# Optimization experiments

Hardware: AMD Instinct MI355X
Metric: run time of the kernel (lower is better)

The kernel has to match this reference:

```python
import jax, jax.numpy as jnp
import numpy as np

# Intersection(mode='product'):
#   a_fk = a @ feats.T            # [Na, K]
#   b_fk = b @ feats.T            # [Nb, K]
#   mask = (a_fk[:,None,:] > 0) & (b_fk[None,:,:] > 0)
#   result = sum_k (a_fk[:,None,:] * b_fk[None,:,:]) * mask   # [Na, Nb]
# For the product op, (x*y)*[x>0 & y>0] == relu(x)*relu(y) elementwise
# (any term with a non-positive factor is zeroed either way), so the
# broadcast+mask+reduce collapses exactly into a GEMM over relu'd scores.

def setup_inputs() -> dict:
    key = jax.random.key(0)
    k1, k2, k3 = jax.random.split(key, 3)
    a = jax.random.normal(k1, (1024, 2048), dtype=jnp.float32)
    b = jax.random.normal(k2, (1024, 2048), dtype=jnp.float32)
    feats = jax.random.normal(k3, (128, 2048), dtype=jnp.float32)
    return {"a": a, "b": b, "feats": feats}

def reference(a, b, feats):
    a_fk = a @ feats.T            # [Na, K]
    b_fk = b @ feats.T            # [Nb, K]
    # masked product-intersection reduced over K; identical math to the
    # broadcast (Na, Nb, K) -> sum formulation of the torch module.
    return jnp.einsum('ak,bk->ab', jax.nn.relu(a_fk), jax.nn.relu(b_fk))
```

## Files before the change

### kernel.cpp

```cpp
#include <hip/hip_runtime.h>


typedef __attribute__((ext_vector_type(8))) __bf16 bf16x8;
typedef __attribute__((ext_vector_type(4))) __bf16 bf16x4;
typedef __attribute__((ext_vector_type(4))) float floatx4;

#define KD     2048
#define NF     128
#define NA     1024
#define NPART  8
#define KSL    256
#define FKN    (2048 * 128)

static __device__ inline bf16x8 cvt8(float4 u, float4 v) {
    bf16x8 s;
    s[0] = (__bf16)u.x; s[1] = (__bf16)u.y; s[2] = (__bf16)u.z; s[3] = (__bf16)u.w;
    s[4] = (__bf16)v.x; s[5] = (__bf16)v.y; s[6] = (__bf16)v.z; s[7] = (__bf16)v.w;
    return s;
}

static __device__ inline bf16x4 cvt4(float4 u) {
    bf16x4 s;
    s[0] = (__bf16)u.x; s[1] = (__bf16)u.y; s[2] = (__bf16)u.z; s[3] = (__bf16)u.w;
    return s;
}

__global__ __launch_bounds__(256) void gemm1_part8(const float* __restrict__ A,
                                                   const float* __restrict__ B,
                                                   const float* __restrict__ F,
                                                   float* __restrict__ part) {
    __shared__ __bf16 Xs[32 * 40];
    __shared__ __bf16 Fs[128 * 40];

    const int t    = threadIdx.x;
    const int m0   = blockIdx.x * 32;
    const int s    = blockIdx.y;
    const int k0   = s * KSL;
    const float* src = (m0 < NA) ? (A + (size_t)m0 * KD)
                                 : (B + (size_t)(m0 - NA) * KD);

    const int lane = t & 63;
    const int w    = t >> 6;
    const int ln   = lane & 15;
    const int quad = lane >> 4;
    const int q8   = quad * 8;

    floatx4 acc[2][2];
#pragma unroll
    for (int mt = 0; mt < 2; mt++)
#pragma unroll
        for (int nt = 0; nt < 2; nt++)
            acc[mt][nt] = (floatx4){0.f, 0.f, 0.f, 0.f};

    const int xrow = t >> 3, xcol = (t & 7) * 4;
    const int frow = t >> 1, fcol = (t & 1) * 16;
    const float* xp = src + (size_t)xrow * KD + (k0 + xcol);
    const float* fp = F   + (size_t)frow * KD + (k0 + fcol);

    float4 xu = *(const float4*)(xp + 0);
    float4 f0 = *(const float4*)(fp + 0);
    float4 f1 = *(const float4*)(fp + 4);
    float4 f2 = *(const float4*)(fp + 8);
    float4 f3 = *(const float4*)(fp + 12);

#pragma unroll
    for (int kk = 0; kk < KSL; kk += 32) {
        *(bf16x4*)&Xs[xrow * 40 + xcol]     = cvt4(xu);
        *(bf16x8*)&Fs[frow * 40 + fcol]     = cvt8(f0, f1);
        *(bf16x8*)&Fs[frow * 40 + fcol + 8] = cvt8(f2, f3);
        __syncthreads();

        if (kk + 32 < KSL) {
            xu = *(const float4*)(xp + kk + 32);
            f0 = *(const float4*)(fp + kk + 32);
            f1 = *(const float4*)(fp + kk + 36);
            f2 = *(const float4*)(fp + kk + 40);
            f3 = *(const float4*)(fp + kk + 44);
        }

        bf16x8 bfrag[2];
#pragma unroll
        for (int nt = 0; nt < 2; nt++)
            bfrag[nt] = *(const bf16x8*)&Fs[(w * 32 + nt * 16 + ln) * 40 + q8];
#pragma unroll
        for (int mt = 0; mt < 2; mt++) {
            bf16x8 af = *(const bf16x8*)&Xs[(mt * 16 + ln) * 40 + q8];
#pragma unroll
            for (int nt = 0; nt < 2; nt++)
                acc[mt][nt] = __builtin_amdgcn_mfma_f32_16x16x32_bf16(
                    af, bfrag[nt], acc[mt][nt], 0, 0, 0);
        }
        __syncthreads();
    }

    float* pdst = part + (size_t)s * FKN;
#pragma unroll
    for (int mt = 0; mt < 2; mt++)
#pragma unroll
        for (int nt = 0; nt < 2; nt++)
#pragma unroll
            for (int r = 0; r < 4; r++) {
                int row = m0 + mt * 16 + quad * 4 + r;
                int col = w * 32 + nt * 16 + ln;
                pdst[(size_t)row * NF + col] = acc[mt][nt][r];
            }
}

__global__ __launch_bounds__(256) void reduce_relu(const float* __restrict__ part,
                                                   __bf16* __restrict__ fkb) {
    int idx = blockIdx.x * 256 + threadIdx.x;
    size_t base = (size_t)idx * 4;
    float4 sum = make_float4(0.f, 0.f, 0.f, 0.f);
#pragma unroll
    for (int s = 0; s < NPART; s++) {
        float4 u = *(const float4*)(part + (size_t)s * FKN + base);
        sum.x += u.x; sum.y += u.y; sum.z += u.z; sum.w += u.w;
    }
    bf16x4 o;
    o[0] = (__bf16)fmaxf(sum.x, 0.f);
    o[1] = (__bf16)fmaxf(sum.y, 0.f);
    o[2] = (__bf16)fmaxf(sum.z, 0.f);
    o[3] = (__bf16)fmaxf(sum.w, 0.f);
    *(bf16x4*)(fkb + base) = o;
}

__global__ __launch_bounds__(256) void gemm2(const __bf16* __restrict__ fkb,
                                             float* __restrict__ out) {
    __shared__ __bf16 Ps[64 * 136];
    __shared__ __bf16 Qs[64 * 136];

    const int t    = threadIdx.x;
    const int i0   = blockIdx.y * 64;
    const int j0   = blockIdx.x * 64;
    const int lane = t & 63;
    const int w    = t >> 6;
    const int wm   = w & 1;
    const int wn   = w >> 1;
    const int ln   = lane & 15;
    const int quad = lane >> 4;
    const int q8   = quad * 8;

    const int prow = t >> 2, pcol = (t & 3) * 32;
    {
        const __bf16* p = fkb + (size_t)(i0 + prow) * NF + pcol;
        const __bf16* q = fkb + (size_t)(NA + j0 + prow) * NF + pcol;
#pragma unroll
        for (int c = 0; c < 32; c += 8) {
            *(bf16x8*)&Ps[prow * 136 + pcol + c] = *(const bf16x8*)(p + c);
            *(bf16x8*)&Qs[prow * 136 + pcol + c] = *(const bf16x8*)(q + c);
        }
    }
    __syncthreads();

    floatx4 acc[2][2];
#pragma unroll
    for (int mt = 0; mt < 2; mt++)
#pragma unroll
        for (int nt = 0; nt < 2; nt++)
            acc[mt][nt] = (floatx4){0.f, 0.f, 0.f, 0.f};

#pragma unroll
    for (int k0 = 0; k0 < 128; k0 += 32) {
        bf16x8 af[2], bf[2];
#pragma unroll
        for (int mt = 0; mt < 2; mt++)
            af[mt] = *(const bf16x8*)&Ps[(wm * 32 + mt * 16 + ln) * 136 + k0 + q8];
#pragma unroll
        for (int nt = 0; nt < 2; nt++)
            bf[nt] = *(const bf16x8*)&Qs[(wn * 32 + nt * 16 + ln) * 136 + k0 + q8];
#pragma unroll
        for (int mt = 0; mt < 2; mt++)
#pragma unroll
            for (int nt = 0; nt < 2; nt++)
                acc[mt][nt] = __builtin_amdgcn_mfma_f32_16x16x32_bf16(
                    af[mt], bf[nt], acc[mt][nt], 0, 0, 0);
    }

#pragma unroll
    for (int mt = 0; mt < 2; mt++)
#pragma unroll
        for (int nt = 0; nt < 2; nt++)
#pragma unroll
            for (int r = 0; r < 4; r++) {
                int row = i0 + wm * 32 + mt * 16 + quad * 4 + r;
                int col = j0 + wn * 32 + nt * 16 + ln;
                out[(size_t)row * 1024 + col] = acc[mt][nt][r];
            }
}

extern "C" void kernel_launch(void* const* d_in, const int* in_sizes, int n_in,
                              void* d_out, int out_size, void* d_ws, size_t ws_size,
                              hipStream_t stream) {
    const float* a     = (const float*)d_in[0];
    const float* b     = (const float*)d_in[1];
    const float* feats = (const float*)d_in[2];
    float* out = (float*)d_out;

    float*   part = (float*)d_ws;
    __bf16*  fkb  = (__bf16*)((char*)d_ws + (size_t)NPART * FKN * 4);

    gemm1_part8<<<dim3(64, NPART), 256, 0, stream>>>(a, b, feats, part);
    reduce_relu<<<256, 256, 0, stream>>>(part, fkb);
    gemm2<<<dim3(16, 16), 256, 0, stream>>>(fkb, out);
}
```

Measured before the change: 79.88 us.

## Fuse split-K reduction and ReLU into GEMM2 and widen GEMM1 k-step

Removes the separate reduce_relu kernel. GEMM2 now sums the 8 split-K partials, applies ReLU and converts to bf16 while staging its tiles into shared memory, which saves one launch and one global round-trip. In exchange every GEMM2 block re-reads fp32 partials for its rows and columns, and each partial is read 16 times across blocks instead of once, which raises L2 traffic. GEMM1 also doubles its per-iteration k-chunk from 32 to 64, halving the number of syncthreads at the cost of more registers for prefetch.

After: 85.81 us. 1.07x slower.

```diff
diff --git a/kernel.cpp b/kernel.cpp
--- a/kernel.cpp
+++ b/kernel.cpp
@@ -19,18 +19,12 @@
     return s;
 }
 
-static __device__ inline bf16x4 cvt4(float4 u) {
-    bf16x4 s;
-    s[0] = (__bf16)u.x; s[1] = (__bf16)u.y; s[2] = (__bf16)u.z; s[3] = (__bf16)u.w;
-    return s;
-}
-
 __global__ __launch_bounds__(256) void gemm1_part8(const float* __restrict__ A,
                                                    const float* __restrict__ B,
                                                    const float* __restrict__ F,
                                                    float* __restrict__ part) {
-    __shared__ __bf16 Xs[32 * 40];
-    __shared__ __bf16 Fs[128 * 40];
+    __shared__ __bf16 Xs[32 * 72];
+    __shared__ __bf16 Fs[128 * 72];
 
     const int t    = threadIdx.x;
     const int m0   = blockIdx.x * 32;
@@ -52,43 +46,47 @@
         for (int nt = 0; nt < 2; nt++)
             acc[mt][nt] = (floatx4){0.f, 0.f, 0.f, 0.f};
 
-    const int xrow = t >> 3, xcol = (t & 7) * 4;
-    const int frow = t >> 1, fcol = (t & 1) * 16;
+    const int xrow = t >> 3, xcol = (t & 7) * 8;
+    const int frow = t >> 1, fcol = (t & 1) * 32;
     const float* xp = src + (size_t)xrow * KD + (k0 + xcol);
     const float* fp = F   + (size_t)frow * KD + (k0 + fcol);
 
-    float4 xu = *(const float4*)(xp + 0);
-    float4 f0 = *(const float4*)(fp + 0);
-    float4 f1 = *(const float4*)(fp + 4);
-    float4 f2 = *(const float4*)(fp + 8);
-    float4 f3 = *(const float4*)(fp + 12);
+    float4 xa = *(const float4*)(xp + 0);
+    float4 xb = *(const float4*)(xp + 4);
+    float4 fa[8];
+#pragma unroll
+    for (int i = 0; i < 8; i++) fa[i] = *(const float4*)(fp + 4 * i);
 
 #pragma unroll
-    for (int kk = 0; kk < KSL; kk += 32) {
-        *(bf16x4*)&Xs[xrow * 40 + xcol]     = cvt4(xu);
-        *(bf16x8*)&Fs[frow * 40 + fcol]     = cvt8(f0, f1);
-        *(bf16x8*)&Fs[frow * 40 + fcol + 8] = cvt8(f2, f3);
+    for (int kk = 0; kk < KSL; kk += 64) {
+        *(bf16x8*)&Xs[xrow * 72 + xcol] = cvt8(xa, xb);
+#pragma unroll
+        for (int i = 0; i < 4; i++)
+            *(bf16x8*)&Fs[frow * 72 + fcol + 8 * i] = cvt8(fa[2 * i], fa[2 * i + 1]);
         __syncthreads();
 
-        if (kk + 32 < KSL) {
-            xu = *(const float4*)(xp + kk + 32);
-            f0 = *(const float4*)(fp + kk + 32);
-            f1 = *(const float4*)(fp + kk + 36);
-            f2 = *(const float4*)(fp + kk + 40);
-            f3 = *(const float4*)(fp + kk + 44);
+        if (kk + 64 < KSL) {
+            xa = *(const float4*)(xp + kk + 64);
+            xb = *(const float4*)(xp + kk + 68);
+#pragma unroll
+            for (int i = 0; i < 8; i++)
+                fa[i] = *(const float4*)(fp + kk + 64 + 4 * i);
         }
 
-        bf16x8 bfrag[2];
 #pragma unroll
-        for (int nt = 0; nt < 2; nt++)
-            bfrag[nt] = *(const bf16x8*)&Fs[(w * 32 + nt * 16 + ln) * 40 + q8];
-#pragma unroll
-        for (int mt = 0; mt < 2; mt++) {
-            bf16x8 af = *(const bf16x8*)&Xs[(mt * 16 + ln) * 40 + q8];
+        for (int sub = 0; sub < 64; sub += 32) {
+            bf16x8 bfrag[2];
 #pragma unroll
             for (int nt = 0; nt < 2; nt++)
-                acc[mt][nt] = __builtin_amdgcn_mfma_f32_16x16x32_bf16(
-                    af, bfrag[nt], acc[mt][nt], 0, 0, 0);
+                bfrag[nt] = *(const bf16x8*)&Fs[(w * 32 + nt * 16 + ln) * 72 + sub + q8];
+#pragma unroll
+            for (int mt = 0; mt < 2; mt++) {
+                bf16x8 af = *(const bf16x8*)&Xs[(mt * 16 + ln) * 72 + sub + q8];
+#pragma unroll
+                for (int nt = 0; nt < 2; nt++)
+                    acc[mt][nt] = __builtin_amdgcn_mfma_f32_16x16x32_bf16(
+                        af, bfrag[nt], acc[mt][nt], 0, 0, 0);
+            }
         }
         __syncthreads();
     }
@@ -106,26 +104,8 @@
             }
 }
 
-__global__ __launch_bounds__(256) void reduce_relu(const float* __restrict__ part,
-                                                   __bf16* __restrict__ fkb) {
-    int idx = blockIdx.x * 256 + threadIdx.x;
-    size_t base = (size_t)idx * 4;
-    float4 sum = make_float4(0.f, 0.f, 0.f, 0.f);
-#pragma unroll
-    for (int s = 0; s < NPART; s++) {
-        float4 u = *(const float4*)(part + (size_t)s * FKN + base);
-        sum.x += u.x; sum.y += u.y; sum.z += u.z; sum.w += u.w;
-    }
-    bf16x4 o;
-    o[0] = (__bf16)fmaxf(sum.x, 0.f);
-    o[1] = (__bf16)fmaxf(sum.y, 0.f);
-    o[2] = (__bf16)fmaxf(sum.z, 0.f);
-    o[3] = (__bf16)fmaxf(sum.w, 0.f);
-    *(bf16x4*)(fkb + base) = o;
-}
-
-__global__ __launch_bounds__(256) void gemm2(const __bf16* __restrict__ fkb,
-                                             float* __restrict__ out) {
+__global__ __launch_bounds__(256) void gemm2_fused(const float* __restrict__ part,
+                                                   float* __restrict__ out) {
     __shared__ __bf16 Ps[64 * 136];
     __shared__ __bf16 Qs[64 * 136];
 
@@ -140,15 +120,29 @@
     const int quad = lane >> 4;
     const int q8   = quad * 8;
 
-    const int prow = t >> 2, pcol = (t & 3) * 32;
-    {
-        const __bf16* p = fkb + (size_t)(i0 + prow) * NF + pcol;
-        const __bf16* q = fkb + (size_t)(NA + j0 + prow) * NF + pcol;
 #pragma unroll
-        for (int c = 0; c < 32; c += 8) {
-            *(bf16x8*)&Ps[prow * 136 + pcol + c] = *(const bf16x8*)(p + c);
-            *(bf16x8*)&Qs[prow * 136 + pcol + c] = *(const bf16x8*)(q + c);
+    for (int g = 0; g < 8; g++) {
+        const int idx4 = g * 256 + t;
+        const int row  = idx4 >> 5;
+        const int col  = (idx4 & 31) * 4;
+        const float* p = part + (size_t)(i0 + row) * NF + col;
+        const float* q = part + (size_t)(NA + j0 + row) * NF + col;
+        float4 sp = make_float4(0.f, 0.f, 0.f, 0.f);
+        float4 sq = make_float4(0.f, 0.f, 0.f, 0.f);
+#pragma unroll
+        for (int s = 0; s < NPART; s++) {
+            float4 u = *(const float4*)(p + (size_t)s * FKN);
+            float4 v = *(const float4*)(q + (size_t)s * FKN);
+            sp.x += u.x; sp.y += u.y; sp.z += u.z; sp.w += u.w;
+            sq.x += v.x; sq.y += v.y; sq.z += v.z; sq.w += v.w;
         }
+        bf16x4 op, oq;
+        op[0] = (__bf16)fmaxf(sp.x, 0.f); op[1] = (__bf16)fmaxf(sp.y, 0.f);
+        op[2] = (__bf16)fmaxf(sp.z, 0.f); op[3] = (__bf16)fmaxf(sp.w, 0.f);
+        oq[0] = (__bf16)fmaxf(sq.x, 0.f); oq[1] = (__bf16)fmaxf(sq.y, 0.f);
+        oq[2] = (__bf16)fmaxf(sq.z, 0.f); oq[3] = (__bf16)fmaxf(sq.w, 0.f);
+        *(bf16x4*)&Ps[row * 136 + col] = op;
+        *(bf16x4*)&Qs[row * 136 + col] = oq;
     }
     __syncthreads();
 
@@ -196,10 +190,8 @@
     const float* feats = (const float*)d_in[2];
     float* out = (float*)d_out;
 
-    float*   part = (float*)d_ws;
-    __bf16*  fkb  = (__bf16*)((char*)d_ws + (size_t)NPART * FKN * 4);
+    float* part = (float*)d_ws;
 
     gemm1_part8<<<dim3(64, NPART), 256, 0, stream>>>(a, b, feats, part);
-    reduce_relu<<<256, 256, 0, stream>>>(part, fkb);
-    gemm2<<<dim3(16, 16), 256, 0, stream>>>(fkb, out);
+    gemm2_fused<<<dim3(16, 16), 256, 0, stream>>>(part, out);
 }
```

## Fuse split-K reduction and ReLU into GEMM1 via last-block atomic counter

Applied to the files above, without the earlier changes.

Removes the separate reduce_relu kernel launch. Each GEMM1 block writes its partial and bumps a per-row-tile atomic counter. The last of the 8 K-split blocks for that tile reads the other partials, adds them to its registers, applies ReLU and writes bf16 output. This saves one launch and one pass over the partial buffer, but puts a serialized tail reduction on the last-arriving blocks and relies on a global counter that is reset at the end of each call.

After: 146.8 us. 83.8% more time.

```diff
diff --git a/kernel.cpp b/kernel.cpp
--- a/kernel.cpp
+++ b/kernel.cpp
@@ -12,6 +12,8 @@
 #define KSL    256
 #define FKN    (2048 * 128)
 
+__device__ int g_ctr[64];
+
 static __device__ inline bf16x8 cvt8(float4 u, float4 v) {
     bf16x8 s;
     s[0] = (__bf16)u.x; s[1] = (__bf16)u.y; s[2] = (__bf16)u.z; s[3] = (__bf16)u.w;
@@ -25,12 +27,14 @@
     return s;
 }
 
-__global__ __launch_bounds__(256) void gemm1_part8(const float* __restrict__ A,
-                                                   const float* __restrict__ B,
-                                                   const float* __restrict__ F,
-                                                   float* __restrict__ part) {
+__global__ __launch_bounds__(256) void gemm1_red(const float* __restrict__ A,
+                                                 const float* __restrict__ B,
+                                                 const float* __restrict__ F,
+                                                 float* __restrict__ part,
+                                                 __bf16* __restrict__ fkb) {
     __shared__ __bf16 Xs[32 * 40];
     __shared__ __bf16 Fs[128 * 40];
+    __shared__ int s_old;
 
     const int t    = threadIdx.x;
     const int m0   = blockIdx.x * 32;
@@ -104,24 +108,42 @@
                 int col = w * 32 + nt * 16 + ln;
                 pdst[(size_t)row * NF + col] = acc[mt][nt][r];
             }
-}
-
-__global__ __launch_bounds__(256) void reduce_relu(const float* __restrict__ part,
-                                                   __bf16* __restrict__ fkb) {
-    int idx = blockIdx.x * 256 + threadIdx.x;
-    size_t base = (size_t)idx * 4;
-    float4 sum = make_float4(0.f, 0.f, 0.f, 0.f);
-#pragma unroll
-    for (int s = 0; s < NPART; s++) {
-        float4 u = *(const float4*)(part + (size_t)s * FKN + base);
-        sum.x += u.x; sum.y += u.y; sum.z += u.z; sum.w += u.w;
-    }
-    bf16x4 o;
-    o[0] = (__bf16)fmaxf(sum.x, 0.f);
-    o[1] = (__bf16)fmaxf(sum.y, 0.f);
-    o[2] = (__bf16)fmaxf(sum.z, 0.f);
-    o[3] = (__bf16)fmaxf(sum.w, 0.f);
-    *(bf16x4*)(fkb + base) = o;
+
+    __threadfence();
+    if (t == 0)
+        s_old = __hip_atomic_fetch_add(&g_ctr[blockIdx.x], 1,
+                                       __ATOMIC_ACQ_REL, __HIP_MEMORY_SCOPE_AGENT);
+    __syncthreads();
+
+    if (s_old == NPART - 1) {
+        __threadfence();
+#pragma unroll
+        for (int s2 = 0; s2 < NPART; s2++) {
+            if (s2 == s) continue;
+            const float* ps = part + (size_t)s2 * FKN;
+#pragma unroll
+            for (int mt = 0; mt < 2; mt++)
+#pragma unroll
+                for (int nt = 0; nt < 2; nt++)
+#pragma unroll
+                    for (int r = 0; r < 4; r++) {
+                        int row = m0 + mt * 16 + quad * 4 + r;
+                        int col = w * 32 + nt * 16 + ln;
+                        acc[mt][nt][r] += ps[(size_t)row * NF + col];
+                    }
+        }
+#pragma unroll
+        for (int mt = 0; mt < 2; mt++)
+#pragma unroll
+            for (int nt = 0; nt < 2; nt++)
+#pragma unroll
+                for (int r = 0; r < 4; r++) {
+                    int row = m0 + mt * 16 + quad * 4 + r;
+                    int col = w * 32 + nt * 16 + ln;
+                    fkb[(size_t)row * NF + col] = (__bf16)fmaxf(acc[mt][nt][r], 0.f);
+                }
+        if (t == 0) atomicExch(&g_ctr[blockIdx.x], 0);
+    }
 }
 
 __global__ __launch_bounds__(256) void gemm2(const __bf16* __restrict__ fkb,
@@ -199,7 +221,6 @@
     float*   part = (float*)d_ws;
     __bf16*  fkb  = (__bf16*)((char*)d_ws + (size_t)NPART * FKN * 4);
 
-    gemm1_part8<<<dim3(64, NPART), 256, 0, stream>>>(a, b, feats, part);
-    reduce_relu<<<256, 256, 0, stream>>>(part, fkb);
+    gemm1_red<<<dim3(64, NPART), 256, 0, stream>>>(a, b, feats, part, fkb);
     gemm2<<<dim3(16, 16), 256, 0, stream>>>(fkb, out);
 }
```

## Fuse split-K reduction and ReLU into the first GEMM with in-block K split

Applied to the files above, without the earlier changes.

Replaces the 8-way grid split-K first GEMM and its separate reduce/ReLU kernel with one kernel. Each 512-thread block computes 16 rows over the full K. Its four wave-pairs each take a K sub-slice, and the partial sums are reduced through shared memory before ReLU and the bf16 store. This drops the fp32 partial buffer round-trip through global memory and one kernel launch. In exchange the grid shrinks to 128 blocks, fewer than the CU count, and every block re-reads the whole feats matrix, which raises L2 traffic and may leave the kernel latency-bound.

Result: slower. 111.8 us (+39.9%).

```diff
diff --git a/kernel.cpp b/kernel.cpp
--- a/kernel.cpp
+++ b/kernel.cpp
@@ -5,12 +5,9 @@
 typedef __attribute__((ext_vector_type(4))) __bf16 bf16x4;
 typedef __attribute__((ext_vector_type(4))) float floatx4;
 
-#define KD     2048
-#define NF     128
-#define NA     1024
-#define NPART  8
-#define KSL    256
-#define FKN    (2048 * 128)
+#define KD   2048
+#define NF   128
+#define NA   1024
 
 static __device__ inline bf16x8 cvt8(float4 u, float4 v) {
     bf16x8 s;
@@ -25,103 +22,87 @@
     return s;
 }
 
-__global__ __launch_bounds__(256) void gemm1_part8(const float* __restrict__ A,
+__global__ __launch_bounds__(512) void gemm1_block(const float* __restrict__ A,
                                                    const float* __restrict__ B,
                                                    const float* __restrict__ F,
-                                                   float* __restrict__ part) {
-    __shared__ __bf16 Xs[32 * 40];
-    __shared__ __bf16 Fs[128 * 40];
+                                                   __bf16* __restrict__ fkb) {
+    __shared__ __attribute__((aligned(16))) __bf16 smem[(16 + 128) * 136];
+    __bf16* Xs = smem;
+    __bf16* Fs = smem + 16 * 136;
 
     const int t    = threadIdx.x;
-    const int m0   = blockIdx.x * 32;
-    const int s    = blockIdx.y;
-    const int k0   = s * KSL;
+    const int m0   = blockIdx.x * 16;
     const float* src = (m0 < NA) ? (A + (size_t)m0 * KD)
                                  : (B + (size_t)(m0 - NA) * KD);
 
     const int lane = t & 63;
     const int w    = t >> 6;
+    const int wf   = w & 1;
+    const int wk   = w >> 1;
     const int ln   = lane & 15;
     const int quad = lane >> 4;
     const int q8   = quad * 8;
+    const int kb   = wk * 32;
 
-    floatx4 acc[2][2];
+    floatx4 acc[4];
 #pragma unroll
-    for (int mt = 0; mt < 2; mt++)
+    for (int nt = 0; nt < 4; nt++) acc[nt] = (floatx4){0.f, 0.f, 0.f, 0.f};
+
+    const int xrow = t >> 5, xcol = (t & 31) * 4;
+    const int frow = t >> 2, fcol = (t & 3) * 32;
+    const float* xp = src + (size_t)xrow * KD + xcol;
+    const float* fp = F   + (size_t)frow * KD + fcol;
+
+    float4 xu = *(const float4*)(xp);
+    float4 fa[8];
 #pragma unroll
-        for (int nt = 0; nt < 2; nt++)
-            acc[mt][nt] = (floatx4){0.f, 0.f, 0.f, 0.f};
+    for (int i = 0; i < 8; i++) fa[i] = *(const float4*)(fp + 4 * i);
 
-    const int xrow = t >> 3, xcol = (t & 7) * 4;
-    const int frow = t >> 1, fcol = (t & 1) * 16;
-    const float* xp = src + (size_t)xrow * KD + (k0 + xcol);
-    const float* fp = F   + (size_t)frow * KD + (k0 + fcol);
-
-    float4 xu = *(const float4*)(xp + 0);
-    float4 f0 = *(const float4*)(fp + 0);
-    float4 f1 = *(const float4*)(fp + 4);
-    float4 f2 = *(const float4*)(fp + 8);
-    float4 f3 = *(const float4*)(fp + 12);
-
+    for (int kk = 0; kk < 16; kk++) {
+        *(bf16x4*)&Xs[xrow * 136 + xcol] = cvt4(xu);
 #pragma unroll
-    for (int kk = 0; kk < KSL; kk += 32) {
-        *(bf16x4*)&Xs[xrow * 40 + xcol]     = cvt4(xu);
-        *(bf16x8*)&Fs[frow * 40 + fcol]     = cvt8(f0, f1);
-        *(bf16x8*)&Fs[frow * 40 + fcol + 8] = cvt8(f2, f3);
+        for (int i = 0; i < 4; i++)
+            *(bf16x8*)&Fs[frow * 136 + fcol + 8 * i] = cvt8(fa[2 * i], fa[2 * i + 1]);
         __syncthreads();
 
-        if (kk + 32 < KSL) {
-            xu = *(const float4*)(xp + kk + 32);
-            f0 = *(const float4*)(fp + kk + 32);
-            f1 = *(const float4*)(fp + kk + 36);
-            f2 = *(const float4*)(fp + kk + 40);
-            f3 = *(const float4*)(fp + kk + 44);
+        if (kk + 1 < 16) {
+            const int g = (kk + 1) * 128;
+            xu = *(const float4*)(xp + g);
+#pragma unroll
+            for (int i = 0; i < 8; i++) fa[i] = *(const float4*)(fp + g + 4 * i);
         }
 
-        bf16x8 bfrag[2];
+        bf16x8 af = *(const bf16x8*)&Xs[ln * 136 + kb + q8];
 #pragma unroll
-        for (int nt = 0; nt < 2; nt++)
-            bfrag[nt] = *(const bf16x8*)&Fs[(w * 32 + nt * 16 + ln) * 40 + q8];
-#pragma unroll
-        for (int mt = 0; mt < 2; mt++) {
-            bf16x8 af = *(const bf16x8*)&Xs[(mt * 16 + ln) * 40 + q8];
-#pragma unroll
-            for (int nt = 0; nt < 2; nt++)
-                acc[mt][nt] = __builtin_amdgcn_mfma_f32_16x16x32_bf16(
-                    af, bfrag[nt], acc[mt][nt], 0, 0, 0);
+        for (int nt = 0; nt < 4; nt++) {
+            bf16x8 bf = *(const bf16x8*)&Fs[(wf * 64 + nt * 16 + ln) * 136 + kb + q8];
+            acc[nt] = __builtin_amdgcn_mfma_f32_16x16x32_bf16(af, bf, acc[nt], 0, 0, 0);
         }
         __syncthreads();
     }
 
-    float* pdst = part + (size_t)s * FKN;
+    float* red = (float*)smem;
+    const int RSTR = 16 * 132;
+    if (wk > 0) {
+        float* rg = red + (size_t)(wk - 1) * RSTR;
 #pragma unroll
-    for (int mt = 0; mt < 2; mt++)
+        for (int nt = 0; nt < 4; nt++)
 #pragma unroll
-        for (int nt = 0; nt < 2; nt++)
+            for (int r = 0; r < 4; r++)
+                rg[(quad * 4 + r) * 132 + wf * 64 + nt * 16 + ln] = acc[nt][r];
+    }
+    __syncthreads();
+    if (wk == 0) {
+#pragma unroll
+        for (int nt = 0; nt < 4; nt++)
 #pragma unroll
             for (int r = 0; r < 4; r++) {
-                int row = m0 + mt * 16 + quad * 4 + r;
-                int col = w * 32 + nt * 16 + ln;
-                pdst[(size_t)row * NF + col] = acc[mt][nt][r];
+                const int ro = (quad * 4 + r) * 132 + wf * 64 + nt * 16 + ln;
+                float v = acc[nt][r] + red[ro] + red[RSTR + ro] + red[2 * RSTR + ro];
+                fkb[(size_t)(m0 + quad * 4 + r) * NF + wf * 64 + nt * 16 + ln] =
+                    (__bf16)fmaxf(v, 0.f);
             }
-}
-
-__global__ __launch_bounds__(256) void reduce_relu(const float* __restrict__ part,
-                                                   __bf16* __restrict__ fkb) {
-    int idx = blockIdx.x * 256 + threadIdx.x;
-    size_t base = (size_t)idx * 4;
-    float4 sum = make_float4(0.f, 0.f, 0.f, 0.f);
-#pragma unroll
-    for (int s = 0; s < NPART; s++) {
-        float4 u = *(const float4*)(part + (size_t)s * FKN + base);
-        sum.x += u.x; sum.y += u.y; sum.z += u.z; sum.w += u.w;
     }
-    bf16x4 o;
-    o[0] = (__bf16)fmaxf(sum.x, 0.f);
-    o[1] = (__bf16)fmaxf(sum.y, 0.f);
-    o[2] = (__bf16)fmaxf(sum.z, 0.f);
-    o[3] = (__bf16)fmaxf(sum.w, 0.f);
-    *(bf16x4*)(fkb + base) = o;
 }
 
 __global__ __launch_bounds__(256) void gemm2(const __bf16* __restrict__ fkb,
@@ -196,10 +177,8 @@
     const float* feats = (const float*)d_in[2];
     float* out = (float*)d_out;
 
-    float*   part = (float*)d_ws;
-    __bf16*  fkb  = (__bf16*)((char*)d_ws + (size_t)NPART * FKN * 4);
+    __bf16* fkb = (__bf16*)d_ws;
 
-    gemm1_part8<<<dim3(64, NPART), 256, 0, stream>>>(a, b, feats, part);
-    reduce_relu<<<256, 256, 0, stream>>>(part, fkb);
+    gemm1_block<<<128, 512, 0, stream>>>(a, b, feats, fkb);
     gemm2<<<dim3(16, 16), 256, 0, stream>>>(fkb, out);
 }
```
